# Optimization experiments

Hardware: AMD Instinct MI355X
Metric: run time of the kernel (lower is better)

The kernel has to match this reference:

```python
import jax, jax.numpy as jnp
import numpy as np

INPUT_SIZE = 5
HIDDEN_SIZE = 10
BATCH = 8192
SEQ_LEN = 512


def setup_inputs() -> dict:
    key = jax.random.key(0)
    ks = jax.random.split(key, 7)
    D, H = INPUT_SIZE, HIDDEN_SIZE
    s_ih = 1.0 / np.sqrt(H)
    x = jax.random.normal(ks[0], (BATCH, SEQ_LEN, D), dtype=jnp.float32)
    # nn.LSTMCell params: weight_ih [4H, D], weight_hh [4H, H], biases [4H]
    W_ih = jax.random.uniform(ks[1], (4 * H, D), jnp.float32, -s_ih, s_ih)
    W_hh = jax.random.uniform(ks[2], (4 * H, H), jnp.float32, -s_ih, s_ih)
    b_ih = jax.random.uniform(ks[3], (4 * H,), jnp.float32, -s_ih, s_ih)
    b_hh = jax.random.uniform(ks[4], (4 * H,), jnp.float32, -s_ih, s_ih)
    # nn.Linear(H, 1)
    W_out = jax.random.uniform(ks[5], (1, H), jnp.float32, -s_ih, s_ih)
    b_out = jax.random.uniform(ks[6], (1,), jnp.float32, -s_ih, s_ih)
    return {"x": x, "W_ih": W_ih, "W_hh": W_hh, "b_ih": b_ih,
            "b_hh": b_hh, "W_out": W_out, "b_out": b_out}


def reference(x, W_ih, W_hh, b_ih, b_hh, W_out, b_out):
    # x: [B, T, D]; per-timestep LSTMCell recurrence, then Linear(H, 1) head.
    B = x.shape[0]
    H = W_hh.shape[1]
    xT = jnp.swapaxes(x, 0, 1)  # [T, B, D]

    def step(carry, xt):
        h, c = carry
        gates = xt @ W_ih.T + b_ih + h @ W_hh.T + b_hh  # [B, 4H]
        i, f, g, o = jnp.split(gates, 4, axis=-1)
        c_new = jax.nn.sigmoid(f) * c + jax.nn.sigmoid(i) * jnp.tanh(g)
        h_new = jax.nn.sigmoid(o) * jnp.tanh(c_new)
        return (h_new, c_new), None

    h0 = jnp.zeros((B, H), dtype=x.dtype)
    c0 = jnp.zeros((B, H), dtype=x.dtype)
    (h_final, _), _ = jax.lax.scan(step, (h0, c0), xT)
    return h_final @ W_out.T + b_out  # [B, 1]
```

## Files before the change

kernel.cpp:

```cpp
#include <hip/hip_runtime.h>


#define BATCH  8192
#define SEQLEN 512
#define INSZ   5
#define HID    10
#define BSTEP  8
#define BV     10

#define L2E  1.442695040888963f
#define L2E2 2.885390081777927f

typedef float     f32x4 __attribute__((ext_vector_type(4)));
typedef _Float16  f16x4 __attribute__((ext_vector_type(4)));
typedef unsigned  u32x2 __attribute__((ext_vector_type(2)));

__device__ __forceinline__ unsigned pkh(float a, float b) {
    return __builtin_bit_cast(unsigned, __builtin_amdgcn_cvt_pkrtz(a, b));
}
__device__ __forceinline__ f16x4 mkab(unsigned lo, unsigned hi) {
    u32x2 t; t.x = lo; t.y = hi;
    return __builtin_bit_cast(f16x4, t);
}
__device__ __forceinline__ f32x4 mfma16(f16x4 a, f16x4 b, f32x4 c) {
    return __builtin_amdgcn_mfma_f32_16x16x16f16(a, b, c, 0, 0, 0);
}
template<int Q>
__device__ __forceinline__ float quadbcast(float v) {
    int r = __builtin_amdgcn_update_dpp(0, __builtin_bit_cast(int, v),
                                        Q * 0x55, 0xF, 0xF, false);
    return __builtin_bit_cast(float, r);
}

__global__ __launch_bounds__(256, 2) void lstm_mfma(
    const float* __restrict__ x,
    const float* __restrict__ Wih,
    const float* __restrict__ Whh,
    const float* __restrict__ bih,
    const float* __restrict__ bhh,
    const float* __restrict__ Wout,
    const float* __restrict__ bout,
    float* __restrict__ out)
{
    const int lane  = threadIdx.x & 63;
    const int wid   = threadIdx.x >> 6;
    const int gwave = (blockIdx.x * blockDim.x + threadIdx.x) >> 6;
    const int col   = lane & 15;
    const int g     = lane >> 4;
    const int q     = col & 3;
    const int sq    = col >> 2;
    const size_t seq = (size_t)gwave * 4 + sq;

    __shared__ unsigned short hsh[4][48];

    const int u = 4 * g + q - 6;
    const bool uvalid = (u >= 0) && (u < HID);

    f16x4 Af[4];
#pragma unroll
    for (int p = 0; p < 4; ++p) {
        const int ug   = 4 * (col >> 2) + p - 6;
        const int gate = col & 3;
        const bool v   = (ug >= 0) && (ug < HID);
        const int uc   = v ? ug : 0;
        const int orow = gate * HID + uc;
        const float sg = (gate == 2) ? L2E2 : -L2E;
        f16x4 a;
#pragma unroll
        for (int e = 0; e < 4; ++e) {
            const int jj = 4 * g + e;
            float w;
            if (jj < 5)       w = Wih[orow * INSZ + jj];
            else if (jj == 5) w = bih[orow] + bhh[orow];
            else              w = Whh[orow * HID + (jj - 6)];
            a[e] = (_Float16)(v ? sg * w : 0.0f);
        }
        Af[p] = a;
    }

    const bool isG0 = (g == 0), isG1 = (g == 1);
    const bool isQ0 = (q == 0), isQ1 = (q == 1), isQ2 = (q == 2), isQ3 = (q == 3);

    const float* xp = x + seq * SEQLEN * INSZ;
    float h  = 0.0f;
    float cs = 0.0f;

    f32x4 bufA[BV], bufB[BV];
    {
        const f32x4* v4 = (const f32x4*)xp;
#pragma unroll
        for (int i = 0; i < BV; ++i) bufA[i] = v4[i];
    }

#define DO_STEP(cx, ss)                                                      \
    {                                                                        \
        const int ixb = (ss) * INSZ;                                         \
        const float xv0 = cx[(ixb + 0) >> 2][(ixb + 0) & 3];                 \
        const float xv1 = cx[(ixb + 1) >> 2][(ixb + 1) & 3];                 \
        const float xv2 = cx[(ixb + 2) >> 2][(ixb + 2) & 3];                 \
        const float xv3 = cx[(ixb + 3) >> 2][(ixb + 3) & 3];                 \
        const float xv4 = cx[(ixb + 4) >> 2][(ixb + 4) & 3];                 \
               \
        const float b0 = quadbcast<0>(h), b1 = quadbcast<1>(h);              \
        const float b2 = quadbcast<2>(h), b3 = quadbcast<3>(h);              \
        const unsigned hA = pkh(b0, b1), hB = pkh(b2, b3);                   \
        const unsigned pairA = isG0 ? pkh(xv0, xv1)                          \
                             : (isG1 ? pkh(xv4, 1.0f) : hA);                 \
        const unsigned pairB = isG0 ? pkh(xv2, xv3) : hB;                    \
        const f16x4 B0 = mkab(isQ0 ? pairA : 0u, isQ0 ? pairB : 0u);         \
        const f16x4 B1 = mkab(isQ1 ? pairA : 0u, isQ1 ? pairB : 0u);         \
        const f16x4 B2 = mkab(isQ2 ? pairA : 0u, isQ2 ? pairB : 0u);         \
        const f16x4 B3 = mkab(isQ3 ? pairA : 0u, isQ3 ? pairB : 0u);         \
        const f32x4 zz = {0.f, 0.f, 0.f, 0.f};                               \
        f32x4 t01 = mfma16(Af[0], B0, zz);                                   \
        t01 = mfma16(Af[1], B1, t01);                                        \
        f32x4 t23 = mfma16(Af[2], B2, zz);                                   \
        t23 = mfma16(Af[3], B3, t23);                                        \
        const f32x4 acc = t01 + t23;                                         \
        const float A_  = __builtin_amdgcn_exp2f(acc[0]);                    \
        const float E1_ = __builtin_amdgcn_exp2f(acc[1]);                    \
        const float U_  = __builtin_amdgcn_exp2f(acc[2]);                    \
        const float Bo_ = __builtin_amdgcn_exp2f(acc[3]);                    \
        const float t1 = 1.0f + A_;                                          \
        const float t2 = 1.0f + E1_;                                         \
        const float t3 = 1.0f + U_;                                          \
        const float um = fmaf(L2E2, U_, -L2E2);            \
        const float m1 = t1 * t3;                                            \
        const float d1 = t2 * m1;                                            \
        const float r1v = __builtin_amdgcn_rcpf(d1);                         \
        const float num = fmaf(cs, m1, um * t2);                             \
        cs = num * r1v;                                                      \
        const float V = __builtin_amdgcn_exp2f(cs);                          \
        const float t4 = 1.0f + Bo_;                                         \
        const float t5 = 1.0f + V;                                           \
        const float r2v = __builtin_amdgcn_rcpf(t4 * t5);                    \
        h = (V - 1.0f) * r2v;                                                \
    }

    for (int it = 0; it < SEQLEN / (2 * BSTEP); ++it) {
        const int tb = it * 2 * BSTEP;
        {
            const f32x4* v4 = (const f32x4*)(xp + (tb + BSTEP) * INSZ);
#pragma unroll
            for (int i = 0; i < BV; ++i) bufB[i] = v4[i];
#pragma unroll
            for (int ss = 0; ss < BSTEP; ++ss) DO_STEP(bufA, ss)
        }
        {
            int nb = tb + 2 * BSTEP;
            if (nb > SEQLEN - BSTEP) nb = SEQLEN - BSTEP;
            const f32x4* v4 = (const f32x4*)(xp + nb * INSZ);
#pragma unroll
            for (int i = 0; i < BV; ++i) bufA[i] = v4[i];
#pragma unroll
            for (int ss = 0; ss < BSTEP; ++ss) DO_STEP(bufB, ss)
        }
    }
#undef DO_STEP

    const int base = sq * 10;
    const int widx = uvalid ? (base + u) : (40 + (lane & 7));
    hsh[wid][widx] = __builtin_bit_cast(unsigned short, (_Float16)h);
    asm volatile("s_waitcnt lgkmcnt(0)" ::: "memory");
    if (g == 0 && q == 0) {
        float r = bout[0];
#pragma unroll
        for (int uu = 0; uu < HID; ++uu) {
            const float hv = (float)__builtin_bit_cast(_Float16, hsh[wid][base + uu]);
            r = fmaf(Wout[uu], hv, r);
        }
        out[gwave * 4 + sq] = r;
    }
}

extern "C" void kernel_launch(void* const* d_in, const int* in_sizes, int n_in,
                              void* d_out, int out_size, void* d_ws, size_t ws_size,
                              hipStream_t stream) {
    const float* x    = (const float*)d_in[0];
    const float* Wih  = (const float*)d_in[1];
    const float* Whh  = (const float*)d_in[2];
    const float* bih  = (const float*)d_in[3];
    const float* bhh  = (const float*)d_in[4];
    const float* Wout = (const float*)d_in[5];
    const float* bout = (const float*)d_in[6];
    float* out = (float*)d_out;

    const int threads = 256;
    const int blocks  = (BATCH * 16) / threads;
    lstm_mfma<<<blocks, threads, 0, stream>>>(x, Wih, Whh, bih, bhh, Wout, bout, out);
}
```

Before: 124.1 us.

## Interleave two independent sequence groups per wave to hide recurrence latency

Each wave now runs two independent LSTM recurrences, for sequences s and s+4096, with their steps interleaved. The aim is instruction-level parallelism, so the MFMA, exp and rcp latency of one chain can overlap the other. The grid is halved, launch bounds drop to one block per SIMD, and the x prefetch chunk shrinks to 4 steps to keep register use in check. The trade-off is half as many waves, so latency hiding between waves falls, along with more register pressure and less prefetch depth.

```diff
diff --git a/kernel.cpp b/kernel.cpp
--- a/kernel.cpp
+++ b/kernel.cpp
@@ -5,8 +5,8 @@
 #define SEQLEN 512
 #define INSZ   5
 #define HID    10
-#define BSTEP  8
-#define BV     10
+#define BSTEP  4
+#define BV     5
 
 #define L2E  1.442695040888963f
 #define L2E2 2.885390081777927f
@@ -32,7 +32,7 @@
     return __builtin_bit_cast(float, r);
 }
 
-__global__ __launch_bounds__(256, 2) void lstm_mfma(
+__global__ __launch_bounds__(256, 1) void lstm_mfma(
     const float* __restrict__ x,
     const float* __restrict__ Wih,
     const float* __restrict__ Whh,
@@ -49,9 +49,10 @@
     const int g     = lane >> 4;
     const int q     = col & 3;
     const int sq    = col >> 2;
-    const size_t seq = (size_t)gwave * 4 + sq;
-
-    __shared__ unsigned short hsh[4][48];
+    const size_t seqA = (size_t)gwave * 4 + sq;
+    const size_t seqB = seqA + 4096;
+
+    __shared__ unsigned short hsh[4][96];
 
     const int u = 4 * g + q - 6;
     const bool uvalid = (u >= 0) && (u < HID);
@@ -81,18 +82,20 @@
     const bool isG0 = (g == 0), isG1 = (g == 1);
     const bool isQ0 = (q == 0), isQ1 = (q == 1), isQ2 = (q == 2), isQ3 = (q == 3);
 
-    const float* xp = x + seq * SEQLEN * INSZ;
-    float h  = 0.0f;
-    float cs = 0.0f;
-
-    f32x4 bufA[BV], bufB[BV];
+    const float* xpA = x + seqA * SEQLEN * INSZ;
+    const float* xpB = x + seqB * SEQLEN * INSZ;
+    float hA = 0.0f, csA = 0.0f;
+    float hB = 0.0f, csB = 0.0f;
+
+    f32x4 a0buf[BV], a1buf[BV], b0buf[BV], b1buf[BV];
     {
-        const f32x4* v4 = (const f32x4*)xp;
-#pragma unroll
-        for (int i = 0; i < BV; ++i) bufA[i] = v4[i];
-    }
-
-#define DO_STEP(cx, ss)                                                      \
+        const f32x4* vA = (const f32x4*)xpA;
+        const f32x4* vB = (const f32x4*)xpB;
+#pragma unroll
+        for (int i = 0; i < BV; ++i) { a0buf[i] = vA[i]; b0buf[i] = vB[i]; }
+    }
+
+#define DO_STEP_G(cx, ss, h, cs)                                             \
     {                                                                        \
         const int ixb = (ss) * INSZ;                                         \
         const float xv0 = cx[(ixb + 0) >> 2][(ixb + 0) & 3];                 \
@@ -100,13 +103,12 @@
         const float xv2 = cx[(ixb + 2) >> 2][(ixb + 2) & 3];                 \
         const float xv3 = cx[(ixb + 3) >> 2][(ixb + 3) & 3];                 \
         const float xv4 = cx[(ixb + 4) >> 2][(ixb + 4) & 3];                 \
-               \
         const float b0 = quadbcast<0>(h), b1 = quadbcast<1>(h);              \
         const float b2 = quadbcast<2>(h), b3 = quadbcast<3>(h);              \
-        const unsigned hA = pkh(b0, b1), hB = pkh(b2, b3);                   \
+        const unsigned hAp = pkh(b0, b1), hBp = pkh(b2, b3);                 \
         const unsigned pairA = isG0 ? pkh(xv0, xv1)                          \
-                             : (isG1 ? pkh(xv4, 1.0f) : hA);                 \
-        const unsigned pairB = isG0 ? pkh(xv2, xv3) : hB;                    \
+                             : (isG1 ? pkh(xv4, 1.0f) : hAp);                \
+        const unsigned pairB = isG0 ? pkh(xv2, xv3) : hBp;                   \
         const f16x4 B0 = mkab(isQ0 ? pairA : 0u, isQ0 ? pairB : 0u);         \
         const f16x4 B1 = mkab(isQ1 ? pairA : 0u, isQ1 ? pairB : 0u);         \
         const f16x4 B2 = mkab(isQ2 ? pairA : 0u, isQ2 ? pairB : 0u);         \
@@ -140,36 +142,49 @@
     for (int it = 0; it < SEQLEN / (2 * BSTEP); ++it) {
         const int tb = it * 2 * BSTEP;
         {
-            const f32x4* v4 = (const f32x4*)(xp + (tb + BSTEP) * INSZ);
-#pragma unroll
-            for (int i = 0; i < BV; ++i) bufB[i] = v4[i];
-#pragma unroll
-            for (int ss = 0; ss < BSTEP; ++ss) DO_STEP(bufA, ss)
+            const f32x4* vA = (const f32x4*)(xpA + (tb + BSTEP) * INSZ);
+            const f32x4* vB = (const f32x4*)(xpB + (tb + BSTEP) * INSZ);
+#pragma unroll
+            for (int i = 0; i < BV; ++i) { a1buf[i] = vA[i]; b1buf[i] = vB[i]; }
+#pragma unroll
+            for (int ss = 0; ss < BSTEP; ++ss) {
+                DO_STEP_G(a0buf, ss, hA, csA)
+                DO_STEP_G(b0buf, ss, hB, csB)
+            }
         }
         {
             int nb = tb + 2 * BSTEP;
             if (nb > SEQLEN - BSTEP) nb = SEQLEN - BSTEP;
-            const f32x4* v4 = (const f32x4*)(xp + nb * INSZ);
-#pragma unroll
-            for (int i = 0; i < BV; ++i) bufA[i] = v4[i];
-#pragma unroll
-            for (int ss = 0; ss < BSTEP; ++ss) DO_STEP(bufB, ss)
-        }
-    }
-#undef DO_STEP
-
-    const int base = sq * 10;
-    const int widx = uvalid ? (base + u) : (40 + (lane & 7));
-    hsh[wid][widx] = __builtin_bit_cast(unsigned short, (_Float16)h);
+            const f32x4* vA = (const f32x4*)(xpA + nb * INSZ);
+            const f32x4* vB = (const f32x4*)(xpB + nb * INSZ);
+#pragma unroll
+            for (int i = 0; i < BV; ++i) { a0buf[i] = vA[i]; b0buf[i] = vB[i]; }
+#pragma unroll
+            for (int ss = 0; ss < BSTEP; ++ss) {
+                DO_STEP_G(a1buf, ss, hA, csA)
+                DO_STEP_G(b1buf, ss, hB, csB)
+            }
+        }
+    }
+#undef DO_STEP_G
+
+    const int baseA = sq * 10;
+    const int baseB = 48 + sq * 10;
+    const int wA = uvalid ? (baseA + u) : (40 + (lane & 7));
+    const int wB = uvalid ? (baseB + u) : (88 + (lane & 7));
+    hsh[wid][wA] = __builtin_bit_cast(unsigned short, (_Float16)hA);
+    hsh[wid][wB] = __builtin_bit_cast(unsigned short, (_Float16)hB);
     asm volatile("s_waitcnt lgkmcnt(0)" ::: "memory");
     if (g == 0 && q == 0) {
-        float r = bout[0];
+        float rA = bout[0], rB = bout[0];
 #pragma unroll
         for (int uu = 0; uu < HID; ++uu) {
-            const float hv = (float)__builtin_bit_cast(_Float16, hsh[wid][base + uu]);
-            r = fmaf(Wout[uu], hv, r);
-        }
-        out[gwave * 4 + sq] = r;
+            const float wv = Wout[uu];
+            rA = fmaf(wv, (float)__builtin_bit_cast(_Float16, hsh[wid][baseA + uu]), rA);
+            rB = fmaf(wv, (float)__builtin_bit_cast(_Float16, hsh[wid][baseB + uu]), rB);
+        }
+        out[seqA] = rA;
+        out[seqB] = rB;
     }
 }
 
@@ -186,6 +201,6 @@
     float* out = (float*)d_out;
 
     const int threads = 256;
-    const int blocks  = (BATCH * 16) / threads;
+    const int blocks  = (BATCH / 8) * 64 / threads;
     lstm_mfma<<<blocks, threads, 0, stream>>>(x, Wih, Whh, bih, bhh, Wout, bout, out);
 }
```

Result: slower. 147.1 us (+18.6%).
